# Performance work log

Measured on AMD Instinct MI355X. Metric: run time of the kernel, lower is better.

## Reference

```python
import jax, jax.numpy as jnp
import numpy as np

DIM = 768
HEADS = 8
DHEAD = 64
DEMB = HEADS * DHEAD  # 512
EPS = 1e-5


def layer_norm(x, g, b):
    mu = jnp.mean(x, axis=-1, keepdims=True)
    var = jnp.var(x, axis=-1, keepdims=True)
    return (x - mu) * jax.lax.rsqrt(var + EPS) * g + b


def setup_inputs() -> dict:
    key = jax.random.key(0)
    ks = jax.random.split(key, 9)
    b, t, n_src, n_ltn = 2, 4, 8192, 64
    inv = 1.0 / np.sqrt(DIM)
    return {
        "src": jax.random.normal(ks[0], (b, t, n_src, DIM), jnp.float32),
        "ltn": jax.random.normal(ks[1], (b, t, n_ltn, DIM), jnp.float32),
        "g_src": jnp.ones((DIM,), jnp.float32),
        "b_src": jnp.zeros((DIM,), jnp.float32),
        "g_ltn": jnp.ones((DIM,), jnp.float32),
        "b_ltn": jnp.zeros((DIM,), jnp.float32),
        # weights stored (in, out) so y = x @ W  (== torch Linear with W.T)
        "Wq": jax.random.normal(ks[2], (DIM, DEMB), jnp.float32) * inv,
        "Wkv": jax.random.normal(ks[3], (DIM, 2 * DEMB), jnp.float32) * inv,
        "Wo": jax.random.normal(ks[4], (DEMB, DIM), jnp.float32) * (1.0 / np.sqrt(DEMB)),
    }


def reference(src, ltn, g_src, b_src, g_ltn, b_ltn, Wq, Wkv, Wo):
    b, t, n_ltn, _ = ltn.shape
    n_src = src.shape[2]
    scale = DHEAD ** -0.5

    src_n = layer_norm(src, g_src, b_src)
    ltn_n = layer_norm(ltn, g_ltn, b_ltn)

    q = ltn_n @ Wq                                  # [b,t,nl,DEMB]
    ctx = jnp.concatenate([src_n, ltn_n], axis=-2)  # [b,t,ns+nl,DIM]
    kv = ctx @ Wkv                                  # [b,t,ns+nl,2*DEMB]
    k, v = jnp.split(kv, 2, axis=-1)

    def to_heads(x):  # b t n (h d) -> b h t n d
        B, T, N, _ = x.shape
        return x.reshape(B, T, N, HEADS, DHEAD).transpose(0, 3, 1, 2, 4)

    q, k, v = to_heads(q), to_heads(k), to_heads(v)

    attn = jnp.einsum('bhtid,bhtjd->bhtij', q, k) * scale
    attn = jax.nn.softmax(attn - jax.lax.stop_gradient(attn.max(axis=-1, keepdims=True)), axis=-1)
    out = jnp.einsum('bhtij,bhtjd->bhtid', attn, v)  # [b,h,t,nl,d]

    out = out.transpose(0, 2, 3, 1, 4).reshape(b, t, n_ltn, DEMB)
    return out @ Wo
```

## Files before the change

### kernel.cpp

```cpp
#include <hip/hip_runtime.h>
#include <hip/hip_bf16.h>
#include <type_traits>


#define N_SRC 8192
#define N_LTN 64
#define N_CTX 8256
#define NBT 8
#define MROWS 66048
#define DIMK 768
#define DEMB 512
#define NSPLIT 16
#define NTILES 65

#define LN_BLOCKS (MROWS / 4)
#define TR_BLOCKS 576
#define KV_BLOCKS 4128
#define Q_BLOCKS  16

typedef short short8 __attribute__((ext_vector_type(8)));
typedef float floatx4 __attribute__((ext_vector_type(4)));
typedef __attribute__((address_space(1))) void gvoid;
typedef __attribute__((address_space(3))) void lvoid;

__device__ inline ushort f2bf(float f) {
    union { float f; unsigned u; } v; v.f = f;
    unsigned u = v.u;
    return (ushort)((u + 0x7fffu + ((u >> 16) & 1u)) >> 16);
}

__global__ __launch_bounds__(256) void prep_kernel(
        const float* __restrict__ src, const float* __restrict__ ltn,
        const float* __restrict__ gs, const float* __restrict__ bs,
        const float* __restrict__ gl, const float* __restrict__ bl,
        ushort* __restrict__ ctx, ushort* __restrict__ qin,
        const float* __restrict__ Wkv, const float* __restrict__ Wq,
        const float* __restrict__ Wo, ushort* __restrict__ WkvT,
        ushort* __restrict__ WqT, ushort* __restrict__ WoT) {
    __shared__ ushort tile[64][65];
    int bid = blockIdx.x;

    if (bid < LN_BLOCKS) {
        int r = bid * 4 + (threadIdx.x >> 6);
        int lane = threadIdx.x & 63;
        int bt = r / N_CTX;
        int i = r - bt * N_CTX;
        const float *x, *g, *b;
        int isl = (i >= N_SRC);
        if (!isl) { x = src + ((size_t)bt * N_SRC + i) * DIMK; g = gs; b = bs; }
        else      { x = ltn + ((size_t)bt * N_LTN + (i - N_SRC)) * DIMK; g = gl; b = bl; }
        float4 v[3]; float s = 0.f, s2 = 0.f;
#pragma unroll
        for (int t = 0; t < 3; t++) {
            float4 xv = *(const float4*)(x + t * 256 + lane * 4);
            v[t] = xv;
            s  += xv.x + xv.y + xv.z + xv.w;
            s2 += xv.x * xv.x + xv.y * xv.y + xv.z * xv.z + xv.w * xv.w;
        }
#pragma unroll
        for (int off = 32; off >= 1; off >>= 1) {
            s  += __shfl_xor(s,  off, 64);
            s2 += __shfl_xor(s2, off, 64);
        }
        float mu  = s * (1.0f / 768.0f);
        float var = s2 * (1.0f / 768.0f) - mu * mu;
        float rs  = rsqrtf(var + 1e-5f);
        ushort* crow = ctx + (size_t)r * DIMK;
        ushort* qrow = isl ? (qin + (size_t)(bt * N_LTN + (i - N_SRC)) * DIMK) : nullptr;
#pragma unroll
        for (int t = 0; t < 3; t++) {
            int idx = t * 256 + lane * 4;
            float4 gv = *(const float4*)(g + idx);
            float4 bv = *(const float4*)(b + idx);
            ushort4 u;
            u.x = f2bf((v[t].x - mu) * rs * gv.x + bv.x);
            u.y = f2bf((v[t].y - mu) * rs * gv.y + bv.y);
            u.z = f2bf((v[t].z - mu) * rs * gv.z + bv.z);
            u.w = f2bf((v[t].w - mu) * rs * gv.w + bv.w);
            *(ushort4*)(crow + idx) = u;
            if (isl) *(ushort4*)(qrow + idx) = u;
        }
        return;
    }

    int bid2 = bid - LN_BLOCKS;
    int z = bid2 / 192;
    int rem = bid2 - z * 192;
    int by = rem >> 4, bx = rem & 15;
    const float* in; ushort* out; int R, C;
    if (z == 0)      { in = Wkv; out = WkvT; R = 768; C = 1024; }
    else if (z == 1) { in = Wq;  out = WqT;  R = 768; C = 512;  }
    else             { in = Wo;  out = WoT;  R = 512; C = 768;  }
    int C0 = bx * 64, R0 = by * 64;
    if (C0 >= C || R0 >= R) return;
    int tc = threadIdx.x & 63, tr4 = threadIdx.x >> 6;
#pragma unroll
    for (int j = 0; j < 16; j++) {
        int r = tr4 + j * 4;
        tile[r][tc] = f2bf(in[(size_t)(R0 + r) * C + C0 + tc]);
    }
    __syncthreads();
#pragma unroll
    for (int j = 0; j < 16; j++) {
        int c = tr4 + j * 4;
        out[(size_t)(C0 + c) * R + R0 + tc] = tile[tc][c];
    }
}

__global__ __launch_bounds__(256) void gemm_kvq(
        const ushort* __restrict__ ctx, const ushort* __restrict__ WkvT,
        ushort* __restrict__ kvb, const ushort* __restrict__ qin,
        const ushort* __restrict__ WqT, ushort* __restrict__ qfb) {
    __shared__ ushort lA[128 * 64];
    __shared__ ushort lB[128 * 64];
    int tid = threadIdx.x;
    int lane = tid & 63, wave = tid >> 6;
    int wm = wave >> 1, wn = wave & 1;

    int lin = blockIdx.x;
    const ushort *A, *B;
    ushort* Cp;
    int bm, bn, N;
    if (lin < KV_BLOCKS) {
        int swz = (lin & 7) * (KV_BLOCKS >> 3) + (lin >> 3);
        bn = swz & 7; bm = swz >> 3;
        A = ctx; B = WkvT; Cp = kvb; N = 1024;
    } else {
        int l2 = lin - KV_BLOCKS;
        bn = l2 & 3; bm = l2 >> 2;
        A = qin; B = WqT; Cp = qfb; N = 512;
    }
    const int K = DIMK;

    floatx4 acc[4][4];
#pragma unroll
    for (int mi = 0; mi < 4; mi++)
#pragma unroll
        for (int ni = 0; ni < 4; ni++) acc[mi][ni] = (floatx4){0.f, 0.f, 0.f, 0.f};

    int srow = lane >> 3;
    int schunk = (lane & 7) ^ srow;
    int quad = lane >> 4, lr = lane & 15;
    const int kiters = K >> 6;

    for (int kt = 0; kt < kiters; kt++) {
#pragma unroll
        for (int c2 = 0; c2 < 4; c2++) {
            int row = c2 * 32 + wave * 8 + srow;
            const ushort* gpA = A + ((size_t)(bm * 128 + row) * K + kt * 64 + schunk * 8);
            ushort* lpA = lA + (c2 * 32 + wave * 8) * 64 + lane * 8;
            __builtin_amdgcn_global_load_lds((gvoid*)gpA, (lvoid*)lpA, 16, 0, 0);
            const ushort* gpB = B + ((size_t)(bn * 128 + row) * K + kt * 64 + schunk * 8);
            ushort* lpB = lB + (c2 * 32 + wave * 8) * 64 + lane * 8;
            __builtin_amdgcn_global_load_lds((gvoid*)gpB, (lvoid*)lpB, 16, 0, 0);
        }
        __syncthreads();
#pragma unroll
        for (int ks = 0; ks < 2; ks++) {
            short8 av[4], bv[4];
            int slot = ((ks * 4 + quad) ^ (lane & 7)) * 8;
#pragma unroll
            for (int mi = 0; mi < 4; mi++)
                av[mi] = *(const short8*)(lA + (wm * 64 + mi * 16 + lr) * 64 + slot);
#pragma unroll
            for (int ni = 0; ni < 4; ni++)
                bv[ni] = *(const short8*)(lB + (wn * 64 + ni * 16 + lr) * 64 + slot);
#pragma unroll
            for (int mi = 0; mi < 4; mi++)
#pragma unroll
                for (int ni = 0; ni < 4; ni++)
                    acc[mi][ni] = __builtin_amdgcn_mfma_f32_16x16x32_bf16(
                        av[mi], bv[ni], acc[mi][ni], 0, 0, 0);
        }
        __syncthreads();
    }
#pragma unroll
    for (int mi = 0; mi < 4; mi++)
#pragma unroll
        for (int ni = 0; ni < 4; ni++)
#pragma unroll
            for (int r = 0; r < 4; r++) {
                int row = bm * 128 + wm * 64 + mi * 16 + quad * 4 + r;
                int col = bn * 128 + wn * 64 + ni * 16 + lr;
                Cp[(size_t)row * N + col] = f2bf(acc[mi][ni][r]);
            }
}

template <typename CT>
__global__ __launch_bounds__(256) void gemm_bt(
        const ushort* __restrict__ A, const ushort* __restrict__ B,
        CT* __restrict__ C, int M, int N, int K) {
    __shared__ ushort lA[128 * 64];
    __shared__ ushort lB[128 * 64];
    int tid = threadIdx.x;
    int lane = tid & 63, wave = tid >> 6;
    int wm = wave >> 1, wn = wave & 1;

    int nwg = gridDim.x * gridDim.y;
    int lin = blockIdx.y * gridDim.x + blockIdx.x;
    int swz = (lin & 7) * (nwg >> 3) + (lin >> 3);
    int bn = swz % gridDim.x, bm = swz / gridDim.x;

    floatx4 acc[4][4];
#pragma unroll
    for (int mi = 0; mi < 4; mi++)
#pragma unroll
        for (int ni = 0; ni < 4; ni++) acc[mi][ni] = (floatx4){0.f, 0.f, 0.f, 0.f};

    int srow = lane >> 3;
    int schunk = (lane & 7) ^ srow;
    int quad = lane >> 4, lr = lane & 15;
    const int kiters = K >> 6;

    for (int kt = 0; kt < kiters; kt++) {
#pragma unroll
        for (int c2 = 0; c2 < 4; c2++) {
            int row = c2 * 32 + wave * 8 + srow;
            const ushort* gpA = A + ((size_t)(bm * 128 + row) * K + kt * 64 + schunk * 8);
            ushort* lpA = lA + (c2 * 32 + wave * 8) * 64 + lane * 8;
            __builtin_amdgcn_global_load_lds((gvoid*)gpA, (lvoid*)lpA, 16, 0, 0);
            const ushort* gpB = B + ((size_t)(bn * 128 + row) * K + kt * 64 + schunk * 8);
            ushort* lpB = lB + (c2 * 32 + wave * 8) * 64 + lane * 8;
            __builtin_amdgcn_global_load_lds((gvoid*)gpB, (lvoid*)lpB, 16, 0, 0);
        }
        __syncthreads();
#pragma unroll
        for (int ks = 0; ks < 2; ks++) {
            short8 av[4], bv[4];
            int slot = ((ks * 4 + quad) ^ (lane & 7)) * 8;
#pragma unroll
            for (int mi = 0; mi < 4; mi++)
                av[mi] = *(const short8*)(lA + (wm * 64 + mi * 16 + lr) * 64 + slot);
#pragma unroll
            for (int ni = 0; ni < 4; ni++)
                bv[ni] = *(const short8*)(lB + (wn * 64 + ni * 16 + lr) * 64 + slot);
#pragma unroll
            for (int mi = 0; mi < 4; mi++)
#pragma unroll
                for (int ni = 0; ni < 4; ni++)
                    acc[mi][ni] = __builtin_amdgcn_mfma_f32_16x16x32_bf16(
                        av[mi], bv[ni], acc[mi][ni], 0, 0, 0);
        }
        __syncthreads();
    }
#pragma unroll
    for (int mi = 0; mi < 4; mi++)
#pragma unroll
        for (int ni = 0; ni < 4; ni++)
#pragma unroll
            for (int r = 0; r < 4; r++) {
                int row = bm * 128 + wm * 64 + mi * 16 + quad * 4 + r;
                int col = bn * 128 + wn * 64 + ni * 16 + lr;
                float vv = acc[mi][ni][r];
                if constexpr (std::is_same<CT, ushort>::value)
                    C[(size_t)row * N + col] = f2bf(vv);
                else
                    C[(size_t)row * N + col] = vv;
            }
}

#define PR 136

__global__ __launch_bounds__(256) void attn_flash(
        const ushort* __restrict__ qfb, const ushort* __restrict__ kvb,
        float* __restrict__ Op, float* __restrict__ ml) {
    __shared__ ushort lK[128 * 64];
    __shared__ ushort lVT[64 * PR];
    __shared__ ushort lP[64 * PR];

    int comb = blockIdx.x, split = blockIdx.y;
    int bt = comb >> 3, h = comb & 7;
    int tid = threadIdx.x;
    int w = tid >> 6, lane = tid & 63, quad = lane >> 4, lr = lane & 15;

    const ushort* kptr = kvb + (size_t)bt * N_CTX * 1024 + h * 64;
    const ushort* vptr = kptr + 512;

    short8 qa[2];
    {
        const ushort* p0 = qfb + (size_t)(bt * 64 + w * 16 + lr) * DEMB + h * 64;
        qa[0] = *(const short8*)(p0 + quad * 8);
        qa[1] = *(const short8*)(p0 + 32 + quad * 8);
    }

    floatx4 accO[4];
#pragma unroll
    for (int nt = 0; nt < 4; nt++) accO[nt] = (floatx4){0.f, 0.f, 0.f, 0.f};
    float m_run[4], l_run[4];
#pragma unroll
    for (int r = 0; r < 4; r++) { m_run[r] = -1e30f; l_run[r] = 0.f; }

    for (int t = split; t < NTILES; t += NSPLIT) {
        int kbase = t * 128;
        __syncthreads();

#pragma unroll
        for (int c2 = 0; c2 < 4; c2++) {
            int jloc = w * 32 + c2 * 8 + (lane >> 3);
            int chunk = (lane & 7) ^ ((lane >> 3) & 7);
            int jg = kbase + jloc; if (jg > N_CTX - 1) jg = N_CTX - 1;
            const ushort* gp = kptr + (size_t)jg * 1024 + chunk * 8;
            ushort* lp = lK + (w * 32 + c2 * 8) * 64 + lane * 8;
            __builtin_amdgcn_global_load_lds((gvoid*)gp, (lvoid*)lp, 16, 0, 0);
        }

        {
            int k0 = kbase + lane * 2;
            bool valid = (k0 + 1) < N_CTX;
            int k0c = valid ? k0 : (N_CTX - 2);
            const ushort* r0 = vptr + (size_t)k0c * 1024 + w * 16;
            const ushort* r1 = r0 + 1024;
            uint4 a0 = *(const uint4*)r0;
            uint4 a1 = *(const uint4*)(r0 + 8);
            uint4 b0 = *(const uint4*)r1;
            uint4 b1 = *(const uint4*)(r1 + 8);
            if (!valid) {
                a0 = make_uint4(0, 0, 0, 0); a1 = a0; b0 = a0; b1 = a0;
            }
            unsigned av8[8] = {a0.x, a0.y, a0.z, a0.w, a1.x, a1.y, a1.z, a1.w};
            unsigned bv8[8] = {b0.x, b0.y, b0.z, b0.w, b1.x, b1.y, b1.z, b1.w};
#pragma unroll
            for (int i = 0; i < 8; i++) {
                unsigned la = av8[i] & 0xffffu, ha = av8[i] >> 16;
                unsigned lb = bv8[i] & 0xffffu, hb = bv8[i] >> 16;
                *(unsigned*)(lVT + (w * 16 + 2 * i) * PR + lane * 2)     = la | (lb << 16);
                *(unsigned*)(lVT + (w * 16 + 2 * i + 1) * PR + lane * 2) = ha | (hb << 16);
            }
        }
        __syncthreads();

        floatx4 accS[8];
#pragma unroll
        for (int nt = 0; nt < 8; nt++) accS[nt] = (floatx4){0.f, 0.f, 0.f, 0.f};
#pragma unroll
        for (int kc = 0; kc < 2; kc++) {
#pragma unroll
            for (int nt = 0; nt < 8; nt++) {
                int kr = nt * 16 + lr;
                int slot = (kc * 4 + quad) ^ (kr & 7);
                short8 bv = *(const short8*)(lK + kr * 64 + slot * 8);
                accS[nt] = __builtin_amdgcn_mfma_f32_16x16x32_bf16(
                    qa[kc], bv, accS[nt], 0, 0, 0);
            }
        }

        float sc[8][4];
        float tmax[4] = {-1e30f, -1e30f, -1e30f, -1e30f};
#pragma unroll
        for (int nt = 0; nt < 8; nt++) {
            bool vk = (kbase + nt * 16 + lr) < N_CTX;
#pragma unroll
            for (int r = 0; r < 4; r++) {
                float s = vk ? accS[nt][r] * 0.125f : -1e30f;
                sc[nt][r] = s;
                tmax[r] = fmaxf(tmax[r], s);
            }
        }
#pragma unroll
        for (int r = 0; r < 4; r++) {
#pragma unroll
            for (int d = 1; d < 16; d <<= 1) tmax[r] = fmaxf(tmax[r], __shfl_xor(tmax[r], d, 64));
        }
        float alpha[4], lsum[4];
#pragma unroll
        for (int r = 0; r < 4; r++) {
            float mn = fmaxf(m_run[r], tmax[r]);
            alpha[r] = __expf(m_run[r] - mn);
            m_run[r] = mn;
            lsum[r] = 0.f;
        }

#pragma unroll
        for (int nt = 0; nt < 8; nt++) {
#pragma unroll
            for (int r = 0; r < 4; r++) {
                float p = __expf(sc[nt][r] - m_run[r]);
                lsum[r] += p;
                lP[(w * 16 + quad * 4 + r) * PR + nt * 16 + lr] = f2bf(p);
            }
        }
#pragma unroll
        for (int r = 0; r < 4; r++) {
#pragma unroll
            for (int d = 1; d < 16; d <<= 1) lsum[r] += __shfl_xor(lsum[r], d, 64);
            l_run[r] = l_run[r] * alpha[r] + lsum[r];
        }
#pragma unroll
        for (int nt = 0; nt < 4; nt++) {
            accO[nt][0] *= alpha[0]; accO[nt][1] *= alpha[1];
            accO[nt][2] *= alpha[2]; accO[nt][3] *= alpha[3];
        }

        short8 av[4];
#pragma unroll
        for (int kc = 0; kc < 4; kc++)
            av[kc] = *(const short8*)(lP + (w * 16 + lr) * PR + kc * 32 + quad * 8);
#pragma unroll
        for (int nt = 0; nt < 4; nt++)
#pragma unroll
            for (int kc = 0; kc < 4; kc++) {
                short8 bv = *(const short8*)(lVT + (nt * 16 + lr) * PR + kc * 32 + quad * 8);
                accO[nt] = __builtin_amdgcn_mfma_f32_16x16x32_bf16(av[kc], bv, accO[nt], 0, 0, 0);
            }
    }

    float* opb = Op + (size_t)(comb * NSPLIT + split) * 64 * 64;
#pragma unroll
    for (int nt = 0; nt < 4; nt++)
#pragma unroll
        for (int r = 0; r < 4; r++)
            opb[(w * 16 + quad * 4 + r) * 64 + nt * 16 + lr] = accO[nt][r];
    if (lr == 0) {
#pragma unroll
        for (int r = 0; r < 4; r++) {
            int row = w * 16 + quad * 4 + r;
            float* mlp = ml + ((size_t)(comb * NSPLIT + split) * 64 + row) * 2;
            mlp[0] = m_run[r]; mlp[1] = l_run[r];
        }
    }
}

__global__ __launch_bounds__(64) void attn_combine(
        const float* __restrict__ Op, const float* __restrict__ ml,
        ushort* __restrict__ outp) {
    int bx = blockIdx.x;
    int comb = bx >> 6, q = bx & 63;
    int bt = comb >> 3, h = comb & 7;
    int d = threadIdx.x;
    float M = -1e30f;
    for (int s = 0; s < NSPLIT; s++)
        M = fmaxf(M, ml[((size_t)(comb * NSPLIT + s) * 64 + q) * 2]);
    float L = 0.f, O = 0.f;
    for (int s = 0; s < NSPLIT; s++) {
        const float* p = ml + ((size_t)(comb * NSPLIT + s) * 64 + q) * 2;
        float wgt = __expf(p[0] - M);
        L = fmaf(wgt, p[1], L);
        O = fmaf(wgt, Op[((size_t)(comb * NSPLIT + s) * 64 + q) * 64 + d], O);
    }
    outp[(size_t)(bt * 64 + q) * DEMB + h * 64 + d] = f2bf(O / L);
}

extern "C" void kernel_launch(void* const* d_in, const int* in_sizes, int n_in,
                              void* d_out, int out_size, void* d_ws, size_t ws_size,
                              hipStream_t stream) {
    const float* src   = (const float*)d_in[0];
    const float* ltn   = (const float*)d_in[1];
    const float* g_src = (const float*)d_in[2];
    const float* b_src = (const float*)d_in[3];
    const float* g_ltn = (const float*)d_in[4];
    const float* b_ltn = (const float*)d_in[5];
    const float* Wq    = (const float*)d_in[6];
    const float* Wkv   = (const float*)d_in[7];
    const float* Wo    = (const float*)d_in[8];
    float* out = (float*)d_out;

    char* ws = (char*)d_ws;
    size_t off = 0;
    auto alloc = [&](size_t bytes) -> void* {
        void* p = ws + off;
        off += (bytes + 255) & ~(size_t)255;
        return p;
    };
    ushort* ctx  = (ushort*)alloc((size_t)MROWS * DIMK * 2);
    ushort* qin  = (ushort*)alloc((size_t)512 * DIMK * 2);
    ushort* WkvT = (ushort*)alloc((size_t)1024 * DIMK * 2);
    ushort* WqT  = (ushort*)alloc((size_t)512 * DIMK * 2);
    ushort* WoT  = (ushort*)alloc((size_t)768 * DEMB * 2);
    ushort* kvb  = (ushort*)alloc((size_t)MROWS * 1024 * 2);
    ushort* qfb  = (ushort*)alloc((size_t)512 * DEMB * 2);
    ushort* outp = (ushort*)alloc((size_t)512 * DEMB * 2);

    float* Op  = (float*)(void*)ctx;
    float* mlb = Op + (size_t)64 * NSPLIT * 64 * 64;

    prep_kernel<<<LN_BLOCKS + TR_BLOCKS, 256, 0, stream>>>(
        src, ltn, g_src, b_src, g_ltn, b_ltn, ctx, qin,
        Wkv, Wq, Wo, WkvT, WqT, WoT);

    gemm_kvq<<<KV_BLOCKS + Q_BLOCKS, 256, 0, stream>>>(
        ctx, WkvT, kvb, qin, WqT, qfb);

    attn_flash<<<dim3(64, NSPLIT), 256, 0, stream>>>(qfb, kvb, Op, mlb);
    attn_combine<<<4096, 64, 0, stream>>>(Op, mlb, outp);

    gemm_bt<float><<<dim3(768 / 128, 512 / 128), 256, 0, stream>>>(
        outp, WoT, out, 512, 768, DEMB);
}
```

Baseline: 508.8 us.

## Fuse split-K attention combine into flash kernel and prefetch V tiles

Removes the separate attn_combine launch by having the last-finishing split block per (bt,head) do the log-sum-exp merge, using an atomic counter zeroed inside gemm_kvq plus threadfence and agent-scope loads. Also folds the 1/sqrt(d) scale into the Q projection epilogue and software-prefetches the next V tile into registers before the QK^T compute. Adds register pressure and a serialized tail combine on one block per head, in exchange for saving a kernel launch and hiding V load latency.

```diff
diff --git a/kernel.cpp b/kernel.cpp
--- a/kernel.cpp
+++ b/kernel.cpp
@@ -27,6 +27,13 @@
     union { float f; unsigned u; } v; v.f = f;
     unsigned u = v.u;
     return (ushort)((u + 0x7fffu + ((u >> 16) & 1u)) >> 16);
+}
+
+__device__ inline float ldag(const float* p) {
+    unsigned u = __hip_atomic_load((const unsigned*)p, __ATOMIC_RELAXED,
+                                   __HIP_MEMORY_SCOPE_AGENT);
+    union { unsigned u; float f; } c; c.u = u;
+    return c.f;
 }
 
 __global__ __launch_bounds__(256) void prep_kernel(
@@ -110,7 +117,8 @@
 __global__ __launch_bounds__(256) void gemm_kvq(
         const ushort* __restrict__ ctx, const ushort* __restrict__ WkvT,
         ushort* __restrict__ kvb, const ushort* __restrict__ qin,
-        const ushort* __restrict__ WqT, ushort* __restrict__ qfb) {
+        const ushort* __restrict__ WqT, ushort* __restrict__ qfb,
+        int* __restrict__ cnt) {
     __shared__ ushort lA[128 * 64];
     __shared__ ushort lB[128 * 64];
     int tid = threadIdx.x;
@@ -121,14 +129,16 @@
     const ushort *A, *B;
     ushort* Cp;
     int bm, bn, N;
+    float scl;
     if (lin < KV_BLOCKS) {
         int swz = (lin & 7) * (KV_BLOCKS >> 3) + (lin >> 3);
         bn = swz & 7; bm = swz >> 3;
-        A = ctx; B = WkvT; Cp = kvb; N = 1024;
+        A = ctx; B = WkvT; Cp = kvb; N = 1024; scl = 1.0f;
     } else {
+        if (lin == KV_BLOCKS && tid < 64) cnt[tid] = 0;
         int l2 = lin - KV_BLOCKS;
         bn = l2 & 3; bm = l2 >> 2;
-        A = qin; B = WqT; Cp = qfb; N = 512;
+        A = qin; B = WqT; Cp = qfb; N = 512; scl = 0.125f;
     }
     const int K = DIMK;
 
@@ -182,7 +192,7 @@
             for (int r = 0; r < 4; r++) {
                 int row = bm * 128 + wm * 64 + mi * 16 + quad * 4 + r;
                 int col = bn * 128 + wn * 64 + ni * 16 + lr;
-                Cp[(size_t)row * N + col] = f2bf(acc[mi][ni][r]);
+                Cp[(size_t)row * N + col] = f2bf(acc[mi][ni][r] * scl);
             }
 }
 
@@ -263,10 +273,12 @@
 
 __global__ __launch_bounds__(256) void attn_flash(
         const ushort* __restrict__ qfb, const ushort* __restrict__ kvb,
-        float* __restrict__ Op, float* __restrict__ ml) {
+        float* __restrict__ Op, float* __restrict__ ml,
+        int* __restrict__ cnt, ushort* __restrict__ outp) {
     __shared__ ushort lK[128 * 64];
     __shared__ ushort lVT[64 * PR];
     __shared__ ushort lP[64 * PR];
+    __shared__ int sLast;
 
     int comb = blockIdx.x, split = blockIdx.y;
     int bt = comb >> 3, h = comb & 7;
@@ -289,6 +301,21 @@
     float m_run[4], l_run[4];
 #pragma unroll
     for (int r = 0; r < 4; r++) { m_run[r] = -1e30f; l_run[r] = 0.f; }
+
+    uint4 vreg[4];
+    unsigned vmask;
+    auto loadV = [&](int t) {
+        int k0 = t * 128 + lane * 2;
+        bool valid = (k0 + 1) < N_CTX;
+        int k0c = valid ? k0 : (N_CTX - 2);
+        const ushort* r0 = vptr + (size_t)k0c * 1024 + w * 16;
+        vreg[0] = *(const uint4*)r0;
+        vreg[1] = *(const uint4*)(r0 + 8);
+        vreg[2] = *(const uint4*)(r0 + 1024);
+        vreg[3] = *(const uint4*)(r0 + 1032);
+        vmask = valid ? 0xffffffffu : 0u;
+    };
+    loadV(split);
 
     for (int t = split; t < NTILES; t += NSPLIT) {
         int kbase = t * 128;
@@ -305,20 +332,14 @@
         }
 
         {
-            int k0 = kbase + lane * 2;
-            bool valid = (k0 + 1) < N_CTX;
-            int k0c = valid ? k0 : (N_CTX - 2);
-            const ushort* r0 = vptr + (size_t)k0c * 1024 + w * 16;
-            const ushort* r1 = r0 + 1024;
-            uint4 a0 = *(const uint4*)r0;
-            uint4 a1 = *(const uint4*)(r0 + 8);
-            uint4 b0 = *(const uint4*)r1;
-            uint4 b1 = *(const uint4*)(r1 + 8);
-            if (!valid) {
-                a0 = make_uint4(0, 0, 0, 0); a1 = a0; b0 = a0; b1 = a0;
-            }
-            unsigned av8[8] = {a0.x, a0.y, a0.z, a0.w, a1.x, a1.y, a1.z, a1.w};
-            unsigned bv8[8] = {b0.x, b0.y, b0.z, b0.w, b1.x, b1.y, b1.z, b1.w};
+            unsigned av8[8] = {vreg[0].x & vmask, vreg[0].y & vmask,
+                               vreg[0].z & vmask, vreg[0].w & vmask,
+                               vreg[1].x & vmask, vreg[1].y & vmask,
+                               vreg[1].z & vmask, vreg[1].w & vmask};
+            unsigned bv8[8] = {vreg[2].x & vmask, vreg[2].y & vmask,
+                               vreg[2].z & vmask, vreg[2].w & vmask,
+                               vreg[3].x & vmask, vreg[3].y & vmask,
+                               vreg[3].z & vmask, vreg[3].w & vmask};
 #pragma unroll
             for (int i = 0; i < 8; i++) {
                 unsigned la = av8[i] & 0xffffu, ha = av8[i] >> 16;
@@ -328,6 +349,9 @@
             }
         }
         __syncthreads();
+
+        int tn = t + NSPLIT;
+        if (tn < NTILES) loadV(tn);
 
         floatx4 accS[8];
 #pragma unroll
@@ -344,15 +368,14 @@
             }
         }
 
-        float sc[8][4];
         float tmax[4] = {-1e30f, -1e30f, -1e30f, -1e30f};
 #pragma unroll
         for (int nt = 0; nt < 8; nt++) {
             bool vk = (kbase + nt * 16 + lr) < N_CTX;
 #pragma unroll
             for (int r = 0; r < 4; r++) {
-                float s = vk ? accS[nt][r] * 0.125f : -1e30f;
-                sc[nt][r] = s;
+                float s = vk ? accS[nt][r] : -1e30f;
+                accS[nt][r] = s;
                 tmax[r] = fmaxf(tmax[r], s);
             }
         }
@@ -374,7 +397,7 @@
         for (int nt = 0; nt < 8; nt++) {
 #pragma unroll
             for (int r = 0; r < 4; r++) {
-                float p = __expf(sc[nt][r] - m_run[r]);
+                float p = __expf(accS[nt][r] - m_run[r]);
                 lsum[r] += p;
                 lP[(w * 16 + quad * 4 + r) * PR + nt * 16 + lr] = f2bf(p);
             }
@@ -418,26 +441,34 @@
             mlp[0] = m_run[r]; mlp[1] = l_run[r];
         }
     }
-}
-
-__global__ __launch_bounds__(64) void attn_combine(
-        const float* __restrict__ Op, const float* __restrict__ ml,
-        ushort* __restrict__ outp) {
-    int bx = blockIdx.x;
-    int comb = bx >> 6, q = bx & 63;
-    int bt = comb >> 3, h = comb & 7;
-    int d = threadIdx.x;
-    float M = -1e30f;
-    for (int s = 0; s < NSPLIT; s++)
-        M = fmaxf(M, ml[((size_t)(comb * NSPLIT + s) * 64 + q) * 2]);
-    float L = 0.f, O = 0.f;
-    for (int s = 0; s < NSPLIT; s++) {
-        const float* p = ml + ((size_t)(comb * NSPLIT + s) * 64 + q) * 2;
-        float wgt = __expf(p[0] - M);
-        L = fmaf(wgt, p[1], L);
-        O = fmaf(wgt, Op[((size_t)(comb * NSPLIT + s) * 64 + q) * 64 + d], O);
-    }
-    outp[(size_t)(bt * 64 + q) * DEMB + h * 64 + d] = f2bf(O / L);
+
+    __threadfence();
+    if (tid == 0)
+        sLast = (atomicAdd(&cnt[comb], 1) == NSPLIT - 1);
+    __syncthreads();
+    if (sLast) {
+        int q = tid >> 2, dg = tid & 3;
+        const float* mlc = ml + ((size_t)(comb * NSPLIT) * 64 + q) * 2;
+        float M = -1e30f;
+        for (int s = 0; s < NSPLIT; s++)
+            M = fmaxf(M, ldag(mlc + s * 128));
+        float L = 0.f;
+        float O[16];
+#pragma unroll
+        for (int j = 0; j < 16; j++) O[j] = 0.f;
+        for (int s = 0; s < NSPLIT; s++) {
+            float m0 = ldag(mlc + s * 128);
+            float l0 = ldag(mlc + s * 128 + 1);
+            float wgt = __expf(m0 - M);
+            L = fmaf(wgt, l0, L);
+            const float* ob = Op + ((size_t)(comb * NSPLIT + s) * 64 + q) * 64 + dg * 16;
+#pragma unroll
+            for (int j = 0; j < 16; j++) O[j] = fmaf(wgt, ldag(ob + j), O[j]);
+        }
+        ushort* op = outp + (size_t)(bt * 64 + q) * DEMB + h * 64 + dg * 16;
+#pragma unroll
+        for (int j = 0; j < 16; j++) op[j] = f2bf(O[j] / L);
+    }
 }
 
 extern "C" void kernel_launch(void* const* d_in, const int* in_sizes, int n_in,
@@ -469,6 +500,7 @@
     ushort* kvb  = (ushort*)alloc((size_t)MROWS * 1024 * 2);
     ushort* qfb  = (ushort*)alloc((size_t)512 * DEMB * 2);
     ushort* outp = (ushort*)alloc((size_t)512 * DEMB * 2);
+    int*    cnt  = (int*)   alloc(64 * sizeof(int));
 
     float* Op  = (float*)(void*)ctx;
     float* mlb = Op + (size_t)64 * NSPLIT * 64 * 64;
@@ -478,10 +510,9 @@
         Wkv, Wq, Wo, WkvT, WqT, WoT);
 
     gemm_kvq<<<KV_BLOCKS + Q_BLOCKS, 256, 0, stream>>>(
-        ctx, WkvT, kvb, qin, WqT, qfb);
-
-    attn_flash<<<dim3(64, NSPLIT), 256, 0, stream>>>(qfb, kvb, Op, mlb);
-    attn_combine<<<4096, 64, 0, stream>>>(Op, mlb, outp);
+        ctx, WkvT, kvb, qin, WqT, qfb, cnt);
+
+    attn_flash<<<dim3(64, NSPLIT), 256, 0, stream>>>(qfb, kvb, Op, mlb, cnt, outp);
 
     gemm_bt<float><<<dim3(768 / 128, 512 / 128), 256, 0, stream>>>(
         outp, WoT, out, 512, 768, DEMB);
```

Result: slower. 712.9 us (+40.1%).
